# Performance work log

Measured on AMD Instinct MI355X. Metric: run time of the kernel, lower is better.

Reference implementation:

```python
import jax, jax.numpy as jnp
import numpy as np

S, B, H, T = 1024, 32, 1024, 512


def setup_inputs() -> dict:
    key = jax.random.key(0)
    ks = jax.random.split(key, 7)
    scale = 1.0 / np.sqrt(H)
    return {
        "hidden": jax.random.normal(ks[0], (S, B, H), dtype=jnp.float32),
        "x": jax.random.normal(ks[1], (B, T, H), dtype=jnp.float32),
        "problem_q": jax.random.normal(ks[2], (B, H), dtype=jnp.float32),
        "K_w": jax.random.normal(ks[3], (H, H), dtype=jnp.float32) * scale,
        "K_b": jax.random.normal(ks[4], (H,), dtype=jnp.float32) * scale,
        "V_w": jax.random.normal(ks[5], (H, H), dtype=jnp.float32) * scale,
        "V_b": jax.random.normal(ks[6], (H,), dtype=jnp.float32) * scale,
    }


def reference(hidden, x, problem_q, K_w, K_b, V_w, V_b):
    # hidden: [S, B, H] -> hidden2: [B, S, H]
    hidden2 = jnp.transpose(hidden, (1, 0, 2))
    # Linear projections (torch Linear: y = x @ W.T + b)
    k = jnp.einsum("bsh,kh->bsk", hidden2, K_w) + K_b  # [B, S, H]
    v = jnp.einsum("bsh,kh->bsk", hidden2, V_w) + V_b  # [B, S, H]
    # scores[b,t,s] = x[b,t] . k[b,s]  (QK^T per batch)
    scores = jnp.einsum("bth,bsh->bts", x, k)
    attn = jax.nn.softmax(scores, axis=-1)  # softmax over encoder positions S
    out = jax.nn.sigmoid(jnp.einsum("bts,bsh->bth", attn, v))  # [B, T, H]
    return out
```

## Files before the change

### kernel.cpp

```cpp
#include <hip/hip_runtime.h>

typedef unsigned short u16;
typedef __attribute__((ext_vector_type(8))) short short8;
typedef __attribute__((ext_vector_type(8))) _Float16 half8;
typedef __attribute__((ext_vector_type(4))) float f32x4;
typedef __attribute__((ext_vector_type(4))) u16 u16x4;
typedef __attribute__((ext_vector_type(4))) unsigned int u32x4;

#define DEVINL static __device__ __forceinline__

DEVINL u16 f2bf(float f) {
  unsigned u = __builtin_bit_cast(unsigned, f);
  u += 0x7fffu + ((u >> 16) & 1u);
  return (u16)(u >> 16);
}
DEVINL float bf2f(u16 h) {
  return __builtin_bit_cast(float, ((unsigned)h) << 16);
}
DEVINL u16 f2h(float f) { return __builtin_bit_cast(u16, (_Float16)f); }
DEVINL float h2f(u16 h) { return (float)__builtin_bit_cast(_Float16, h); }

DEVINL void gload16(const void* g, void* l) {
  __builtin_amdgcn_global_load_lds(
      (const __attribute__((address_space(1))) void*)g,
      (__attribute__((address_space(3))) void*)l, 16, 0, 0);
}

#define BAR() asm volatile("s_barrier" ::: "memory")
#define WAIT_VMN(n) asm volatile("s_waitcnt vmcnt(" #n ")" ::: "memory")
#define WAIT_VM_LGKM0() asm volatile("s_waitcnt vmcnt(0) lgkmcnt(0)" ::: "memory")


__global__ __launch_bounds__(512) void cvt_hidden2_k(const float* __restrict__ hid,
                                                     u16* __restrict__ hf,
                                                     u16* __restrict__ hT) {
  __shared__ u16 tl[64][136];
  const int s0 = blockIdx.x * 64;
  const int h0 = blockIdx.y * 128;
  const int b = blockIdx.z;
  const int t = threadIdx.x;
  const int r = t >> 5;
  const int c4 = (t & 31) * 4;
#pragma unroll
  for (int it = 0; it < 4; ++it) {
    const int s = it * 16 + r;
    const f32x4 v = *(const f32x4*)(hid + ((size_t)(s0 + s) * 32 + b) * 1024 + h0 + c4);
    u16x4 of;
    const int cs = c4 ^ (it << 2);
#pragma unroll
    for (int j = 0; j < 4; ++j) {
      of[j] = f2h(v[j]);
      tl[s][cs + j] = f2bf(v[j]);
    }
    *(u16x4*)(hf + ((size_t)b * 1024 + s0 + s) * 1024 + h0 + c4) = of;
  }
  __syncthreads();
  const int h = t >> 2;
  const int sq = (t & 3) * 16;
  u16 tmp[16] __attribute__((aligned(16)));
#pragma unroll
  for (int i = 0; i < 16; ++i)
    tmp[i] = tl[sq + i][h ^ ((((sq + i) >> 4) & 3) << 2)];
  u16* dst = hT + ((size_t)b * 1024 + h0 + h) * 1024 + s0 + sq;
  *(u32x4*)(dst) = *(const u32x4*)&tmp[0];
  *(u32x4*)(dst + 8) = *(const u32x4*)&tmp[8];
}

__global__ __launch_bounds__(256) void cvt_f32_bf16_k(const float* __restrict__ in,
                                                      u16* __restrict__ out, long n4) {
  long i = (long)blockIdx.x * 256 + threadIdx.x;
  const long stride = (long)gridDim.x * 256;
  for (; i < n4; i += stride) {
    const f32x4 v = ((const f32x4*)in)[i];
    u16x4 o;
#pragma unroll
    for (int j = 0; j < 4; ++j) o[j] = f2bf(v[j]);
    ((u16x4*)out)[i] = o;
  }
}

__global__ __launch_bounds__(256) void cvt_w_t_h_k(const float* __restrict__ in,
                                                   u16* __restrict__ out) {
  __shared__ float tile[64][65];
  const int bh = blockIdx.x * 64;
  const int bj = blockIdx.y * 64;
  const int t = threadIdx.x;
  const int r = t >> 4;
  const int c4 = (t & 15) * 4;
#pragma unroll
  for (int it = 0; it < 4; ++it) {
    const int row = it * 16 + r;
    const f32x4 v = *(const f32x4*)(in + (size_t)(bj + row) * 1024 + bh + c4);
#pragma unroll
    for (int j = 0; j < 4; ++j) tile[c4 + j][row] = v[j];
  }
  __syncthreads();
#pragma unroll
  for (int it = 0; it < 4; ++it) {
    const int hrow = it * 16 + r;
    u16x4 of;
#pragma unroll
    for (int j = 0; j < 4; ++j) of[j] = f2h(tile[hrow][c4 + j]);
    *(u16x4*)(out + (size_t)(bh + hrow) * 1024 + bj + c4) = of;
  }
}

__global__ __launch_bounds__(512) void gemm_qp_k(
    const float* __restrict__ X, const u16* __restrict__ Bm,
    u16* __restrict__ Chi, u16* __restrict__ Clo) {
  __shared__ u16 lA[2][256 * 64];
  __shared__ u16 lB[2][256 * 32];
  const int bid = blockIdx.x;
  const int swz = (bid & 7) * 32 + (bid >> 3);
  const int m0 = (swz >> 2) * 256;
  const int n0 = (swz & 3) * 256;
  const int tid = threadIdx.x;
  const int lane = tid & 63, wid = tid >> 6;
  const int wr = wid >> 2, wc = wid & 3;
  const int fr = lane & 15, fk = lane >> 4;

  f32x4 acc[8][4] = {};

#define STAGEAF(pb, kt)                                                        \
  {                                                                            \
    _Pragma("unroll") for (int j = 0; j < 2; ++j) {                            \
      const int ps = j * 512 + tid;                                            \
      const int r = ps >> 2, q = ps & 3;                                       \
      const float* src = X + (size_t)(m0 + r) * 1024 + (kt) * 32 + q * 8;      \
      const f32x4 v0 = *(const f32x4*)src;                                     \
      const f32x4 v1 = *(const f32x4*)(src + 4);                               \
      short8 hs, ls;                                                           \
      _Pragma("unroll") for (int e = 0; e < 4; ++e) {                          \
        const u16 a0 = f2h(v0[e]);                                             \
        const u16 a1 = f2h(v1[e]);                                             \
        hs[e] = (short)a0;                                                     \
        hs[e + 4] = (short)a1;                                                 \
        ls[e] = (short)f2h(v0[e] - h2f(a0));                                   \
        ls[e + 4] = (short)f2h(v1[e] - h2f(a1));                               \
      }                                                                        \
      const int c = q ^ (r & 7);                                               \
      *(short8*)&lA[pb][r * 64 + c * 8] = hs;                                  \
      *(short8*)&lA[pb][r * 64 + (c ^ 4) * 8] = ls;                            \
    }                                                                          \
  }
#define STAGEB(pb, kt)                                                         \
  {                                                                            \
    _Pragma("unroll") for (int j = 0; j < 2; ++j) {                            \
      const int slot = j * 512 + tid;                                          \
      const int r = slot >> 2;                                                 \
      const int g = (slot & 3) ^ ((r >> 1) & 3);                               \
      gload16(Bm + (size_t)(n0 + r) * 1024 + (kt) * 32 + g * 8,                \
              &lB[pb][(j * 512 + wid * 64) * 8]);                              \
    }                                                                          \
  }

  STAGEAF(0, 0);
  STAGEB(0, 0);

  for (int t = 0; t < 32; ++t) {
    const int p = t & 1;
    WAIT_VM_LGKM0();
    BAR();
    half8 bf[4];
#pragma unroll
    for (int nf = 0; nf < 4; ++nf) {
      const int rn = wc * 64 + nf * 16 + fr;
      const int cn = fk ^ ((rn >> 1) & 3);
      bf[nf] = *(const half8*)&lB[p][rn * 32 + cn * 8];
    }
    if (t < 31) {
      STAGEB(p ^ 1, t + 1);
      STAGEAF(p ^ 1, t + 1);
    }
#pragma unroll
    for (int ph = 0; ph < 4; ++ph) {
      half8 ah[2], al[2];
#pragma unroll
      for (int i = 0; i < 2; ++i) {
        const int r = wr * 128 + (ph * 2 + i) * 16 + fr;
        const int ch = fk ^ (r & 7);
        ah[i] = *(const half8*)&lA[p][r * 64 + ch * 8];
        al[i] = *(const half8*)&lA[p][r * 64 + (ch ^ 4) * 8];
      }
      __builtin_amdgcn_s_setprio(1);
#pragma unroll
      for (int i = 0; i < 2; ++i)
#pragma unroll
        for (int nf = 0; nf < 4; ++nf) {
          acc[ph * 2 + i][nf] =
              __builtin_amdgcn_mfma_f32_16x16x32_f16(ah[i], bf[nf], acc[ph * 2 + i][nf], 0, 0, 0);
          acc[ph * 2 + i][nf] =
              __builtin_amdgcn_mfma_f32_16x16x32_f16(al[i], bf[nf], acc[ph * 2 + i][nf], 0, 0, 0);
        }
      __builtin_amdgcn_s_setprio(0);
    }
  }
#undef STAGEAF
#undef STAGEB

  const int cb = n0 + wc * 64 + fr;
  const int rb = m0 + wr * 128 + fk * 4;
#pragma unroll
  for (int mf = 0; mf < 8; ++mf)
#pragma unroll
    for (int nf = 0; nf < 4; ++nf) {
      const int col = cb + nf * 16;
#pragma unroll
      for (int j = 0; j < 4; ++j) {
        const int row = rb + mf * 16 + j;
        const float kv = acc[mf][nf][j];
        const u16 hi = f2h(kv);
        Chi[(size_t)row * 1024 + col] = hi;
        Clo[(size_t)row * 1024 + col] = f2h(kv - h2f(hi));
      }
    }
}

__global__ __launch_bounds__(512) void gemm_sc_k(
    const u16* __restrict__ Qh_, const u16* __restrict__ Ql_,
    const u16* __restrict__ Hf_, float* __restrict__ S) {
  __shared__ u16 lA[2][128 * 128];
  __shared__ u16 lB[2][256 * 64];
  const int bid = blockIdx.x;
  const int swz = (bid & 7) * 64 + (bid >> 3);
  const int z = swz >> 4;
  const int m0 = ((swz >> 2) & 3) * 128;
  const int n0 = (swz & 3) * 256;
  const u16* Ah = Qh_ + (size_t)z * 512 * 1024;
  const u16* Al = Ql_ + (size_t)z * 512 * 1024;
  const u16* Bm = Hf_ + (size_t)z * 1024 * 1024;
  float* Cf = S + (size_t)z * 512 * 1024;
  const int tid = threadIdx.x;
  const int lane = tid & 63, wid = tid >> 6;
  const int wr = wid >> 2, wc = wid & 3;
  const int fr = lane & 15, fk = lane >> 4;

  f32x4 acc[4][4] = {};

#define STAGEA(pb, kt)                                                         \
  {                                                                            \
    _Pragma("unroll") for (int j = 0; j < 4; ++j) {                            \
      const int slot = j * 512 + tid;                                          \
      const int r = slot >> 4;                                                 \
      const int g = (slot & 15) ^ (r & 7);                                     \
      const u16* src = (g < 8) ? Ah : Al;                                      \
      gload16(src + (size_t)(m0 + r) * 1024 + (kt) * 64 + (g & 7) * 8,         \
              &lA[pb][slot * 8]);                                              \
    }                                                                          \
  }
#define STAGEB(pb, kt)                                                         \
  {                                                                            \
    _Pragma("unroll") for (int j = 0; j < 4; ++j) {                            \
      const int slot = j * 512 + tid;                                          \
      const int r = slot >> 3;                                                 \
      const int g = (slot & 7) ^ (r & 7);                                      \
      gload16(Bm + (size_t)(n0 + r) * 1024 + (kt) * 64 + g * 8,                \
              &lB[pb][slot * 8]);                                              \
    }                                                                          \
  }

  STAGEA(0, 0);
  STAGEB(0, 0);

  for (int t = 0; t < 16; ++t) {
    const int p = t & 1;
    WAIT_VMN(0);
    BAR();
    half8 bf[4][2];
#pragma unroll
    for (int nf = 0; nf < 4; ++nf) {
      const int rn = wc * 64 + nf * 16 + fr;
#pragma unroll
      for (int ks = 0; ks < 2; ++ks) {
        const int c = (ks * 4 + fk) ^ (rn & 7);
        bf[nf][ks] = *(const half8*)&lB[p][rn * 64 + c * 8];
      }
    }
    if (t < 15) {
      STAGEA(p ^ 1, t + 1);
      STAGEB(p ^ 1, t + 1);
    }
#pragma unroll
    for (int mf = 0; mf < 4; ++mf) {
      const int r = wr * 64 + mf * 16 + fr;
      half8 ah[2], al[2];
#pragma unroll
      for (int ks = 0; ks < 2; ++ks) {
        const int kc = ks * 4 + fk;
        const int ch = kc ^ (r & 7);
        ah[ks] = *(const half8*)&lA[p][r * 128 + ch * 8];
        al[ks] = *(const half8*)&lA[p][r * 128 + (ch + 8) * 8];
      }
      __builtin_amdgcn_s_setprio(1);
#pragma unroll
      for (int nf = 0; nf < 4; ++nf)
#pragma unroll
        for (int ks = 0; ks < 2; ++ks) {
          acc[mf][nf] = __builtin_amdgcn_mfma_f32_16x16x32_f16(
              ah[ks], bf[nf][ks], acc[mf][nf], 0, 0, 0);
          acc[mf][nf] = __builtin_amdgcn_mfma_f32_16x16x32_f16(
              al[ks], bf[nf][ks], acc[mf][nf], 0, 0, 0);
        }
      __builtin_amdgcn_s_setprio(0);
    }
  }
#undef STAGEA
#undef STAGEB

  const int cb = n0 + wc * 64 + fr;
  const int rb = m0 + wr * 64 + fk * 4;
#pragma unroll
  for (int mf = 0; mf < 4; ++mf)
#pragma unroll
    for (int nf = 0; nf < 4; ++nf) {
      const int col = cb + nf * 16;
#pragma unroll
      for (int j = 0; j < 4; ++j) {
        const int row = rb + mf * 16 + j;
        Cf[(size_t)row * 1024 + col] = acc[mf][nf][j];
      }
    }
}

template <int CM>
__global__ __launch_bounds__(512) void gemm1_8ph_k(
    const u16* __restrict__ A_, const u16* __restrict__ Bt_,
    const float* __restrict__ bias, void* __restrict__ Cout) {
  __shared__ u16 lds[2][2][256 * 64];
  const int bid = blockIdx.x;
  const int swz = (bid & 7) * 32 + (bid >> 3);
  int m0, n0;
  const u16 *A, *Bt;
  float* Cf = nullptr;
  u16* Cb = nullptr;
  if (CM == 0) {
    const int z = swz >> 3;
    m0 = ((swz >> 2) & 1) * 256;
    n0 = (swz & 3) * 256;
    A = A_ + (size_t)z * 512 * 1024;
    Bt = Bt_ + (size_t)z * 1024 * 1024;
    Cb = (u16*)Cout + (size_t)z * 512 * 1024;
  } else {
    m0 = (swz >> 2) * 256;
    n0 = (swz & 3) * 256;
    A = A_; Bt = Bt_;
    Cf = (float*)Cout;
  }
  const int tid = threadIdx.x;
  const int lane = tid & 63, wid = tid >> 6;
  const int wr = wid >> 2, wc = wid & 3;
  const int fr = lane & 15, fk = lane >> 4;

  f32x4 acc[8][4] = {};

#define STAGE1(pb, q, gp, rb, kt)                                              \
  {                                                                            \
    _Pragma("unroll") for (int j = 0; j < 4; ++j) {                            \
      const int slot = j * 512 + tid;                                          \
      const int r = slot >> 3;                                                 \
      const int g = (slot & 7) ^ (r & 7);                                      \
      gload16((gp) + (size_t)((rb) + r) * 1024 + (kt) * 64 + g * 8,            \
              &lds[pb][q][(j * 512 + wid * 64) * 8]);                          \
    }                                                                          \
  }

  STAGE1(0, 0, A, m0, 0);
  STAGE1(0, 1, Bt, n0, 0);

  for (int t = 0; t < 16; ++t) {
    const int p = t & 1;
    WAIT_VMN(0);
    BAR();
    short8 bfr[4][2];
#pragma unroll
    for (int nf = 0; nf < 4; ++nf) {
      const int rn = wc * 64 + nf * 16 + fr;
#pragma unroll
      for (int ks = 0; ks < 2; ++ks) {
        const int g = (ks * 4 + fk) ^ (rn & 7);
        bfr[nf][ks] = *(const short8*)&lds[p][1][rn * 64 + g * 8];
      }
    }
    if (t < 15) {
      STAGE1(p ^ 1, 0, A, m0, t + 1);
      STAGE1(p ^ 1, 1, Bt, n0, t + 1);
    }
#pragma unroll
    for (int ph = 0; ph < 4; ++ph) {
      short8 a[2][2];
#pragma unroll
      for (int i = 0; i < 2; ++i) {
        const int r = wr * 128 + (ph * 2 + i) * 16 + fr;
#pragma unroll
        for (int ks = 0; ks < 2; ++ks) {
          const int g = (ks * 4 + fk) ^ (r & 7);
          a[i][ks] = *(const short8*)&lds[p][0][r * 64 + g * 8];
        }
      }
      __builtin_amdgcn_s_setprio(1);
#pragma unroll
      for (int i = 0; i < 2; ++i)
#pragma unroll
        for (int nf = 0; nf < 4; ++nf) {
          acc[ph * 2 + i][nf] = __builtin_amdgcn_mfma_f32_16x16x32_bf16(
              a[i][0], bfr[nf][0], acc[ph * 2 + i][nf], 0, 0, 0);
          acc[ph * 2 + i][nf] = __builtin_amdgcn_mfma_f32_16x16x32_bf16(
              a[i][1], bfr[nf][1], acc[ph * 2 + i][nf], 0, 0, 0);
        }
      __builtin_amdgcn_s_setprio(0);
    }
  }
#undef STAGE1

  const int cb = n0 + wc * 64 + fr;
  const int rb = m0 + wr * 128 + fk * 4;
  if (CM == 0) {
#pragma unroll
    for (int mf = 0; mf < 8; ++mf)
#pragma unroll
      for (int nf = 0; nf < 4; ++nf) {
        const int col = cb + nf * 16;
#pragma unroll
        for (int j = 0; j < 4; ++j) {
          const int row = rb + mf * 16 + j;
          Cb[(size_t)row * 1024 + col] = f2bf(acc[mf][nf][j]);
        }
      }
  } else {
#pragma unroll
    for (int mf = 0; mf < 8; ++mf)
#pragma unroll
      for (int nf = 0; nf < 4; ++nf) {
        const int col = cb + nf * 16;
        const float bv = bias[col];
#pragma unroll
        for (int j = 0; j < 4; ++j) {
          const int row = rb + mf * 16 + j;
          const float xv = acc[mf][nf][j] + bv;
          Cf[(size_t)row * 1024 + col] = 1.0f / (1.0f + __expf(-xv));
        }
      }
  }
}

__global__ __launch_bounds__(256) void softmax_k(const float* __restrict__ S,
                                                 u16* __restrict__ Attn) {
  const float* rp = S + (size_t)blockIdx.x * 1024;
  const int tid = threadIdx.x;
  const int lane = tid & 63, wid = tid >> 6;
  const f32x4 v = ((const f32x4*)rp)[tid];
  float mx = fmaxf(fmaxf(v[0], v[1]), fmaxf(v[2], v[3]));
#pragma unroll
  for (int off = 32; off; off >>= 1) mx = fmaxf(mx, __shfl_xor(mx, off));
  __shared__ float red[4];
  __shared__ float red2[4];
  if (lane == 0) red[wid] = mx;
  __syncthreads();
  mx = fmaxf(fmaxf(red[0], red[1]), fmaxf(red[2], red[3]));
  const float e0 = __expf(v[0] - mx), e1 = __expf(v[1] - mx);
  const float e2 = __expf(v[2] - mx), e3 = __expf(v[3] - mx);
  float s = (e0 + e1) + (e2 + e3);
#pragma unroll
  for (int off = 32; off; off >>= 1) s += __shfl_xor(s, off);
  if (lane == 0) red2[wid] = s;
  __syncthreads();
  const float inv = 1.0f / (red2[0] + red2[1] + red2[2] + red2[3]);
  u16x4 o;
  o[0] = f2bf(e0 * inv); o[1] = f2bf(e1 * inv); o[2] = f2bf(e2 * inv); o[3] = f2bf(e3 * inv);
  ((u16x4*)(Attn + (size_t)blockIdx.x * 1024))[tid] = o;
}

extern "C" void kernel_launch(void* const* d_in, const int* in_sizes, int n_in,
                              void* d_out, int out_size, void* d_ws, size_t ws_size,
                              hipStream_t stream) {
  const float* hidden = (const float*)d_in[0];
  const float* x = (const float*)d_in[1];
  const float* K_w = (const float*)d_in[3];
  const float* V_w = (const float*)d_in[5];
  const float* V_b = (const float*)d_in[6];

  char* ws = (char*)d_ws;
  u16* hf16 = (u16*)(ws);
  u16* hT = (u16*)(ws + 67108864);
  u16* qhi = (u16*)(ws + 134217728);
  u16* qlo = (u16*)(ws + 167772160);
  float* scoresF = (float*)(ws + 201326592);
  u16* attn = hf16;
  u16* ctx = qhi;
  u16* kwT = (u16*)(ws + 268435456);
  u16* vw = kwT + 1024 * 1024;
  float* out = (float*)d_out;

  cvt_hidden2_k<<<dim3(16, 8, 32), 512, 0, stream>>>(hidden, hf16, hT);
  cvt_w_t_h_k<<<dim3(16, 16), 256, 0, stream>>>(K_w, kwT);
  cvt_f32_bf16_k<<<1024, 256, 0, stream>>>(V_w, vw, 1024L * 1024 / 4);
  gemm_qp_k<<<256, 512, 0, stream>>>(x, kwT, qhi, qlo);
  gemm_sc_k<<<512, 512, 0, stream>>>(qhi, qlo, hf16, scoresF);
  softmax_k<<<16384, 256, 0, stream>>>(scoresF, attn);
  gemm1_8ph_k<0><<<256, 512, 0, stream>>>(attn, hT, nullptr, ctx);
  gemm1_8ph_k<1><<<256, 512, 0, stream>>>(ctx, vw, V_b, out);
}
```

Before: 335.1 us.

## Fuse score GEMM with row softmax, computing full 1024-wide rows per block

The score GEMM and the separate softmax kernel are merged: each block now computes a 64x1024 strip of scores (all encoder positions for 64 query rows), then does the row max/sum reductions in registers and LDS and writes bf16 attention directly. This removes the round trip of the fp32 score matrix through global memory and one kernel launch. In exchange the tile shape changes (K step 32, a larger B tile in LDS, 256 blocks instead of 512), which lowers the parallelism and adds extra barriers for the reductions.

New measurement: 321.4 us. -4.1%, faster.

```diff
diff --git a/kernel.cpp b/kernel.cpp
--- a/kernel.cpp
+++ b/kernel.cpp
@@ -216,109 +216,149 @@
     }
 }
 
-__global__ __launch_bounds__(512) void gemm_sc_k(
+__global__ __launch_bounds__(512) void gemm_sc_fused_k(
     const u16* __restrict__ Qh_, const u16* __restrict__ Ql_,
-    const u16* __restrict__ Hf_, float* __restrict__ S) {
-  __shared__ u16 lA[2][128 * 128];
-  __shared__ u16 lB[2][256 * 64];
+    const u16* __restrict__ Hf_, u16* __restrict__ Attn) {
+  __shared__ u16 lA[2][64 * 64];
+  __shared__ u16 lB[2][1024 * 32];
+  __shared__ float red[8][64];
+  __shared__ float grow[64];
   const int bid = blockIdx.x;
-  const int swz = (bid & 7) * 64 + (bid >> 3);
-  const int z = swz >> 4;
-  const int m0 = ((swz >> 2) & 3) * 128;
-  const int n0 = (swz & 3) * 256;
-  const u16* Ah = Qh_ + (size_t)z * 512 * 1024;
-  const u16* Al = Ql_ + (size_t)z * 512 * 1024;
+  const int swz = (bid & 7) * 32 + (bid >> 3);
+  const int z = swz >> 3;
+  const int m0 = (swz & 7) * 64;
+  const u16* Ah = Qh_ + (size_t)z * 512 * 1024 + (size_t)m0 * 1024;
+  const u16* Al = Ql_ + (size_t)z * 512 * 1024 + (size_t)m0 * 1024;
   const u16* Bm = Hf_ + (size_t)z * 1024 * 1024;
-  float* Cf = S + (size_t)z * 512 * 1024;
+  u16* Ao = Attn + (size_t)z * 512 * 1024 + (size_t)m0 * 1024;
   const int tid = threadIdx.x;
   const int lane = tid & 63, wid = tid >> 6;
-  const int wr = wid >> 2, wc = wid & 3;
   const int fr = lane & 15, fk = lane >> 4;
 
-  f32x4 acc[4][4] = {};
+  f32x4 acc[4][8] = {};
 
 #define STAGEA(pb, kt)                                                         \
   {                                                                            \
-    _Pragma("unroll") for (int j = 0; j < 4; ++j) {                            \
-      const int slot = j * 512 + tid;                                          \
-      const int r = slot >> 4;                                                 \
-      const int g = (slot & 15) ^ (r & 7);                                     \
-      const u16* src = (g < 8) ? Ah : Al;                                      \
-      gload16(src + (size_t)(m0 + r) * 1024 + (kt) * 64 + (g & 7) * 8,         \
-              &lA[pb][slot * 8]);                                              \
-    }                                                                          \
+    const int r = tid >> 3;                                                    \
+    const int g = (tid & 7) ^ (r & 7);                                         \
+    const u16* src = (g < 4) ? Ah : Al;                                        \
+    gload16(src + (size_t)r * 1024 + (kt) * 32 + (g & 3) * 8,                  \
+            &lA[pb][(wid * 64) * 8]);                                          \
   }
 #define STAGEB(pb, kt)                                                         \
   {                                                                            \
-    _Pragma("unroll") for (int j = 0; j < 4; ++j) {                            \
+    _Pragma("unroll") for (int j = 0; j < 8; ++j) {                            \
       const int slot = j * 512 + tid;                                          \
-      const int r = slot >> 3;                                                 \
-      const int g = (slot & 7) ^ (r & 7);                                      \
-      gload16(Bm + (size_t)(n0 + r) * 1024 + (kt) * 64 + g * 8,                \
-              &lB[pb][slot * 8]);                                              \
+      const int r = slot >> 2;                                                 \
+      const int g = (slot & 3) ^ ((r >> 1) & 3);                               \
+      gload16(Bm + (size_t)r * 1024 + (kt) * 32 + g * 8,                       \
+              &lB[pb][(j * 512 + wid * 64) * 8]);                              \
     }                                                                          \
   }
 
   STAGEA(0, 0);
   STAGEB(0, 0);
 
-  for (int t = 0; t < 16; ++t) {
+  for (int t = 0; t < 32; ++t) {
     const int p = t & 1;
     WAIT_VMN(0);
     BAR();
-    half8 bf[4][2];
-#pragma unroll
-    for (int nf = 0; nf < 4; ++nf) {
-      const int rn = wc * 64 + nf * 16 + fr;
-#pragma unroll
-      for (int ks = 0; ks < 2; ++ks) {
-        const int c = (ks * 4 + fk) ^ (rn & 7);
-        bf[nf][ks] = *(const half8*)&lB[p][rn * 64 + c * 8];
-      }
-    }
-    if (t < 15) {
+    half8 bf[8];
+#pragma unroll
+    for (int nf = 0; nf < 8; ++nf) {
+      const int rn = wid * 128 + nf * 16 + fr;
+      const int cn = fk ^ ((rn >> 1) & 3);
+      bf[nf] = *(const half8*)&lB[p][rn * 32 + cn * 8];
+    }
+    if (t < 31) {
       STAGEA(p ^ 1, t + 1);
       STAGEB(p ^ 1, t + 1);
     }
 #pragma unroll
     for (int mf = 0; mf < 4; ++mf) {
-      const int r = wr * 64 + mf * 16 + fr;
-      half8 ah[2], al[2];
-#pragma unroll
-      for (int ks = 0; ks < 2; ++ks) {
-        const int kc = ks * 4 + fk;
-        const int ch = kc ^ (r & 7);
-        ah[ks] = *(const half8*)&lA[p][r * 128 + ch * 8];
-        al[ks] = *(const half8*)&lA[p][r * 128 + (ch + 8) * 8];
-      }
+      const int r = mf * 16 + fr;
+      const int ch = fk ^ (r & 7);
+      const half8 ah = *(const half8*)&lA[p][r * 64 + ch * 8];
+      const half8 al = *(const half8*)&lA[p][r * 64 + (ch ^ 4) * 8];
       __builtin_amdgcn_s_setprio(1);
 #pragma unroll
-      for (int nf = 0; nf < 4; ++nf)
-#pragma unroll
-        for (int ks = 0; ks < 2; ++ks) {
-          acc[mf][nf] = __builtin_amdgcn_mfma_f32_16x16x32_f16(
-              ah[ks], bf[nf][ks], acc[mf][nf], 0, 0, 0);
-          acc[mf][nf] = __builtin_amdgcn_mfma_f32_16x16x32_f16(
-              al[ks], bf[nf][ks], acc[mf][nf], 0, 0, 0);
-        }
+      for (int nf = 0; nf < 8; ++nf) {
+        acc[mf][nf] = __builtin_amdgcn_mfma_f32_16x16x32_f16(ah, bf[nf], acc[mf][nf], 0, 0, 0);
+        acc[mf][nf] = __builtin_amdgcn_mfma_f32_16x16x32_f16(al, bf[nf], acc[mf][nf], 0, 0, 0);
+      }
       __builtin_amdgcn_s_setprio(0);
     }
   }
 #undef STAGEA
 #undef STAGEB
 
-  const int cb = n0 + wc * 64 + fr;
-  const int rb = m0 + wr * 64 + fk * 4;
+  float m16[4][4];
 #pragma unroll
   for (int mf = 0; mf < 4; ++mf)
 #pragma unroll
-    for (int nf = 0; nf < 4; ++nf) {
-      const int col = cb + nf * 16;
-#pragma unroll
-      for (int j = 0; j < 4; ++j) {
-        const int row = rb + mf * 16 + j;
-        Cf[(size_t)row * 1024 + col] = acc[mf][nf][j];
-      }
+    for (int j = 0; j < 4; ++j) {
+      float m = acc[mf][0][j];
+#pragma unroll
+      for (int nf = 1; nf < 8; ++nf) m = fmaxf(m, acc[mf][nf][j]);
+#pragma unroll
+      for (int off = 1; off < 16; off <<= 1) m = fmaxf(m, __shfl_xor(m, off));
+      m16[mf][j] = m;
+    }
+  if (fr == 0) {
+#pragma unroll
+    for (int mf = 0; mf < 4; ++mf)
+#pragma unroll
+      for (int j = 0; j < 4; ++j) red[wid][mf * 16 + fk * 4 + j] = m16[mf][j];
+  }
+  __syncthreads();
+  if (wid == 0 && lane < 64) {
+    float g = red[0][lane];
+#pragma unroll
+    for (int w = 1; w < 8; ++w) g = fmaxf(g, red[w][lane]);
+    grow[lane] = g;
+  }
+  __syncthreads();
+#pragma unroll
+  for (int mf = 0; mf < 4; ++mf)
+#pragma unroll
+    for (int j = 0; j < 4; ++j) {
+      const float gm = grow[mf * 16 + fk * 4 + j];
+      float s = 0.f;
+#pragma unroll
+      for (int nf = 0; nf < 8; ++nf) {
+        const float e = __expf(acc[mf][nf][j] - gm);
+        acc[mf][nf][j] = e;
+        s += e;
+      }
+#pragma unroll
+      for (int off = 1; off < 16; off <<= 1) s += __shfl_xor(s, off);
+      m16[mf][j] = s;
+    }
+  __syncthreads();
+  if (fr == 0) {
+#pragma unroll
+    for (int mf = 0; mf < 4; ++mf)
+#pragma unroll
+      for (int j = 0; j < 4; ++j) red[wid][mf * 16 + fk * 4 + j] = m16[mf][j];
+  }
+  __syncthreads();
+  if (wid == 0 && lane < 64) {
+    float g = red[0][lane];
+#pragma unroll
+    for (int w = 1; w < 8; ++w) g += red[w][lane];
+    grow[lane] = 1.0f / g;
+  }
+  __syncthreads();
+#pragma unroll
+  for (int mf = 0; mf < 4; ++mf)
+#pragma unroll
+    for (int j = 0; j < 4; ++j) {
+      const int lr = mf * 16 + fk * 4 + j;
+      const float inv = grow[lr];
+      u16* rowp = Ao + (size_t)lr * 1024;
+#pragma unroll
+      for (int nf = 0; nf < 8; ++nf)
+        rowp[wid * 128 + nf * 16 + fr] = f2bf(acc[mf][nf][j] * inv);
     }
 }
 
@@ -443,33 +483,6 @@
   }
 }
 
-__global__ __launch_bounds__(256) void softmax_k(const float* __restrict__ S,
-                                                 u16* __restrict__ Attn) {
-  const float* rp = S + (size_t)blockIdx.x * 1024;
-  const int tid = threadIdx.x;
-  const int lane = tid & 63, wid = tid >> 6;
-  const f32x4 v = ((const f32x4*)rp)[tid];
-  float mx = fmaxf(fmaxf(v[0], v[1]), fmaxf(v[2], v[3]));
-#pragma unroll
-  for (int off = 32; off; off >>= 1) mx = fmaxf(mx, __shfl_xor(mx, off));
-  __shared__ float red[4];
-  __shared__ float red2[4];
-  if (lane == 0) red[wid] = mx;
-  __syncthreads();
-  mx = fmaxf(fmaxf(red[0], red[1]), fmaxf(red[2], red[3]));
-  const float e0 = __expf(v[0] - mx), e1 = __expf(v[1] - mx);
-  const float e2 = __expf(v[2] - mx), e3 = __expf(v[3] - mx);
-  float s = (e0 + e1) + (e2 + e3);
-#pragma unroll
-  for (int off = 32; off; off >>= 1) s += __shfl_xor(s, off);
-  if (lane == 0) red2[wid] = s;
-  __syncthreads();
-  const float inv = 1.0f / (red2[0] + red2[1] + red2[2] + red2[3]);
-  u16x4 o;
-  o[0] = f2bf(e0 * inv); o[1] = f2bf(e1 * inv); o[2] = f2bf(e2 * inv); o[3] = f2bf(e3 * inv);
-  ((u16x4*)(Attn + (size_t)blockIdx.x * 1024))[tid] = o;
-}
-
 extern "C" void kernel_launch(void* const* d_in, const int* in_sizes, int n_in,
                               void* d_out, int out_size, void* d_ws, size_t ws_size,
                               hipStream_t stream) {
@@ -484,8 +497,7 @@
   u16* hT = (u16*)(ws + 67108864);
   u16* qhi = (u16*)(ws + 134217728);
   u16* qlo = (u16*)(ws + 167772160);
-  float* scoresF = (float*)(ws + 201326592);
-  u16* attn = hf16;
+  u16* attn = (u16*)(ws + 201326592);
   u16* ctx = qhi;
   u16* kwT = (u16*)(ws + 268435456);
   u16* vw = kwT + 1024 * 1024;
@@ -495,8 +507,7 @@
   cvt_w_t_h_k<<<dim3(16, 16), 256, 0, stream>>>(K_w, kwT);
   cvt_f32_bf16_k<<<1024, 256, 0, stream>>>(V_w, vw, 1024L * 1024 / 4);
   gemm_qp_k<<<256, 512, 0, stream>>>(x, kwT, qhi, qlo);
-  gemm_sc_k<<<512, 512, 0, stream>>>(qhi, qlo, hf16, scoresF);
-  softmax_k<<<16384, 256, 0, stream>>>(scoresF, attn);
+  gemm_sc_fused_k<<<256, 512, 0, stream>>>(qhi, qlo, hf16, attn);
   gemm1_8ph_k<0><<<256, 512, 0, stream>>>(attn, hT, nullptr, ctx);
   gemm1_8ph_k<1><<<256, 512, 0, stream>>>(ctx, vw, V_b, out);
 }
```
